# Performance work log

Measured on AMD Instinct MI355X. Metric: run time of the kernel, lower is better.

The kernel has to match this reference:

```python
import jax, jax.numpy as jnp
import numpy as np

N = 50000        # nodes
E = 1600000      # edges (avg degree 32)
CZ = 64          # c_z pair channel dim
STEPS = 3        # num_equilibration_steps
DITHER = 1e-4    # dither_eps in average_rotations


def quat_mul(a, b):
    # Hamilton product, quats as [w, x, y, z]
    aw, ax, ay, az = a[..., 0], a[..., 1], a[..., 2], a[..., 3]
    bw, bx, by, bz = b[..., 0], b[..., 1], b[..., 2], b[..., 3]
    return jnp.stack([
        aw * bw - ax * bx - ay * by - az * bz,
        aw * bx + ax * bw + ay * bz - az * by,
        aw * by - ax * bz + ay * bw + az * bx,
        aw * bz + ax * by - ay * bx + az * bw,
    ], axis=-1)


def quat_conj(q):
    return q * jnp.array([1.0, -1.0, -1.0, -1.0], q.dtype)


def quat_to_rot(q):
    w, x, y, z = q[..., 0], q[..., 1], q[..., 2], q[..., 3]
    r00 = 1 - 2 * (y * y + z * z); r01 = 2 * (x * y - w * z); r02 = 2 * (x * z + w * y)
    r10 = 2 * (x * y + w * z); r11 = 1 - 2 * (x * x + z * z); r12 = 2 * (y * z - w * x)
    r20 = 2 * (x * z - w * y); r21 = 2 * (y * z + w * x); r22 = 1 - 2 * (x * x + y * y)
    return jnp.stack([
        jnp.stack([r00, r01, r02], -1),
        jnp.stack([r10, r11, r12], -1),
        jnp.stack([r20, r21, r22], -1),
    ], axis=-2)


def rotmat_to_quat(R):
    # Branchless Shepperd method: 4 candidates, pick numerically best.
    m00, m01, m02 = R[..., 0, 0], R[..., 0, 1], R[..., 0, 2]
    m10, m11, m12 = R[..., 1, 0], R[..., 1, 1], R[..., 1, 2]
    m20, m21, m22 = R[..., 2, 0], R[..., 2, 1], R[..., 2, 2]
    q0 = jnp.stack([1 + m00 + m11 + m22, m21 - m12, m02 - m20, m10 - m01], -1)
    q1 = jnp.stack([m21 - m12, 1 + m00 - m11 - m22, m01 + m10, m02 + m20], -1)
    q2 = jnp.stack([m02 - m20, m01 + m10, 1 - m00 + m11 - m22, m12 + m21], -1)
    q3 = jnp.stack([m10 - m01, m02 + m20, m12 + m21, 1 - m00 - m11 + m22], -1)
    cand = jnp.stack([q0, q1, q2, q3], axis=-2)           # [N,4,4]
    scores = jnp.stack([m00 + m11 + m22, m00, m11, m22], -1)
    idx = jnp.argmax(scores, axis=-1)
    q = cand[jnp.arange(cand.shape[0]), idx]              # [N,4]
    q = q / jnp.linalg.norm(q, axis=-1, keepdims=True)
    return q * jnp.where(q[..., :1] < 0, -1.0, 1.0)      # canonical w >= 0


def rotmat_to_rotvec(R):
    q = rotmat_to_quat(R)
    w, v = q[..., 0], q[..., 1:]
    vn = jnp.linalg.norm(v, axis=-1)
    theta = 2.0 * jnp.arctan2(vn, w)
    small = vn < 1e-6
    safe = jnp.where(small, 1.0, vn)
    return jnp.where(small[..., None], 2.0 * v, (theta / safe)[..., None] * v)


def rotvec_to_quat(rotvec, eps=1e-8):
    theta = jnp.linalg.norm(rotvec + eps, axis=-1)
    omega = rotvec / theta[..., None]
    return jnp.concatenate([jnp.cos(theta / 2)[..., None],
                            jnp.sin(theta / 2)[..., None] * omega], axis=-1)


def setup_inputs() -> dict:
    key = jax.random.key(0)
    ks = jax.random.split(key, 8)
    return {
        "edge_features": jax.random.normal(ks[0], (E, CZ), jnp.float32),
        "quats": jax.random.normal(ks[1], (N, 4), jnp.float32),
        "trans": jax.random.normal(ks[2], (N, 3), jnp.float32) * 10.0,
        "W_update": jax.random.normal(ks[3], (CZ, 6), jnp.float32) * 0.02,
        "b_update": jax.random.normal(ks[4], (6,), jnp.float32) * 0.02,
        "W_logits": jax.random.normal(ks[5], (CZ, 1), jnp.float32) * 0.1,
        "b_logits": jax.random.normal(ks[6], (1,), jnp.float32) * 0.1,
        "edge_index": jax.random.randint(ks[7], (2, E), 0, N, jnp.int32),
    }


def reference(edge_features, quats, trans, W_update, b_update, W_logits, b_logits, edge_index):
    n = quats.shape[0]
    dst, src = edge_index[0], edge_index[1]

    # pairwise update vec + segment softmax weights over destination node (edge_index[1])
    q_upd = edge_features @ W_update + b_update              # [E,6]
    logits = edge_features @ W_logits + b_logits             # [E,1]
    seg_max = jax.ops.segment_max(logits, src, num_segments=n)
    seg_max = jnp.where(jnp.isfinite(seg_max), seg_max, 0.0)
    ex = jnp.exp(logits - seg_max[src])
    denom = jax.ops.segment_sum(ex, src, num_segments=n)
    weights = ex / (denom[src] + 1e-16)                      # [E,1]

    # relative rigid: inv(dst) o src
    qn = quats / jnp.linalg.norm(quats, axis=-1, keepdims=True)
    Rn = quat_to_rot(qn)                                     # [N,3,3]
    q_rel = quat_mul(quat_conj(qn[dst]), qn[src])            # [E,4]
    t_rel = jnp.einsum('eji,ej->ei', Rn[dst], trans[src] - trans[dst])  # R^T (t_s - t_d)

    # compose_q_update_vec (openfold): q' = q + q*(0,b,c,d), normalized; t' = t + R(q) t_vec
    bcd, tvec = q_upd[:, :3], q_upd[:, 3:]
    pair_q = q_rel + quat_mul(q_rel, jnp.concatenate([jnp.zeros_like(bcd[:, :1]), bcd], -1))
    pair_q = pair_q / jnp.linalg.norm(pair_q, axis=-1, keepdims=True)
    pair_t = t_rel + jnp.einsum('eij,ej->ei', quat_to_rot(q_rel), tvec)
    pair_R = quat_to_rot(pair_q)                             # [E,3,3]

    # equilibrate loop: scatter rotation averaging with SVD projection
    R, t = Rn, trans
    key = jax.random.key(42)
    for step in range(STEPS):
        dst_R, dst_t = R[dst], t[dst]
        R_pred = jnp.einsum('eij,ejk->eik', dst_R, pair_R)   # [E,3,3]
        R_sum = jax.ops.segment_sum((R_pred * weights[:, :, None]).reshape(-1, 9),
                                    src, num_segments=n).reshape(n, 3, 3)
        R_sum = R_sum + DITHER * jax.random.normal(jax.random.fold_in(key, step),
                                                   R_sum.shape, R_sum.dtype)
        U, S, Vh = jnp.linalg.svd(R_sum, full_matrices=False)
        d = jnp.linalg.det(U @ Vh)
        col = jnp.stack([jnp.ones_like(d), jnp.ones_like(d), d], -1)[:, None, :]
        R = U @ (Vh * col)                                   # proper rotation
        t_pred = dst_t + jnp.einsum('eij,ej->ei', dst_R, pair_t)
        t = jax.ops.segment_sum(t_pred * weights, src, num_segments=n)

    q_out = rotvec_to_quat(rotmat_to_rotvec(R))
    return jnp.concatenate([q_out, t], axis=-1)              # [N,7]
```

## Files before the change

kernel.cpp:

```cpp
#include <hip/hip_runtime.h>
#include <math.h>

#define TPB 256
#define SCAN_B 1024

__device__ __forceinline__ void quat_to_R(float w, float x, float y, float z, float* R) {
    R[0] = 1.f - 2.f*(y*y + z*z);
    R[1] = 2.f*(x*y - w*z);
    R[2] = 2.f*(x*z + w*y);
    R[3] = 2.f*(x*y + w*z);
    R[4] = 1.f - 2.f*(x*x + z*z);
    R[5] = 2.f*(y*z - w*x);
    R[6] = 2.f*(x*z - w*y);
    R[7] = 2.f*(y*z + w*x);
    R[8] = 1.f - 2.f*(x*x + y*y);
}

__device__ __forceinline__ float hsum32(float v) {
    #pragma unroll
    for (int o = 16; o > 0; o >>= 1) v += __shfl_xor(v, o);
    return v;
}
__device__ __forceinline__ float hmax32(float v) {
    #pragma unroll
    for (int o = 16; o > 0; o >>= 1) v = fmaxf(v, __shfl_xor(v, o));
    return v;
}

__global__ __launch_bounds__(TPB) void k_init(
    const float* __restrict__ quats, const float* __restrict__ trans,
    float* __restrict__ qn, float* __restrict__ RT, int* __restrict__ deg, int N)
{
    int n = blockIdx.x * TPB + threadIdx.x;
    if (n >= N) return;
    float4 q = ((const float4*)quats)[n];
    float inv = rsqrtf(q.x*q.x + q.y*q.y + q.z*q.z + q.w*q.w);
    float w = q.x*inv, x = q.y*inv, y = q.z*inv, z = q.w*inv;
    ((float4*)qn)[n] = make_float4(w, x, y, z);
    float R[9];
    quat_to_R(w, x, y, z, R);
    float t0 = trans[(size_t)n*3+0], t1 = trans[(size_t)n*3+1], t2 = trans[(size_t)n*3+2];
    float4* rt = (float4*)(RT + (size_t)n*12);
    rt[0] = make_float4(R[0], R[1], R[2], t0);
    rt[1] = make_float4(R[3], R[4], R[5], t1);
    rt[2] = make_float4(R[6], R[7], R[8], t2);
    deg[n] = 0;
}

__global__ __launch_bounds__(TPB) void k_hist(
    const int* __restrict__ ei, int* __restrict__ deg, int E)
{
    int e = blockIdx.x * TPB + threadIdx.x;
    if (e >= E) return;
    atomicAdd(deg + ei[(size_t)E + e], 1);
}

__global__ __launch_bounds__(SCAN_B) void k_scan1(
    const int* __restrict__ deg, int* __restrict__ row, int* __restrict__ bsum, int N)
{
    __shared__ int sh[SCAN_B];
    int i = blockIdx.x * SCAN_B + threadIdx.x;
    int v = (i < N) ? deg[i] : 0;
    sh[threadIdx.x] = v;
    __syncthreads();
    #pragma unroll
    for (int o = 1; o < SCAN_B; o <<= 1) {
        int t = (threadIdx.x >= o) ? sh[threadIdx.x - o] : 0;
        __syncthreads();
        sh[threadIdx.x] += t;
        __syncthreads();
    }
    if (i < N) row[i] = sh[threadIdx.x] - v;
    if (threadIdx.x == SCAN_B - 1) bsum[blockIdx.x] = sh[SCAN_B - 1];
}

__global__ __launch_bounds__(SCAN_B) void k_scan2(int* __restrict__ bsum, int nb)
{
    __shared__ int sh[SCAN_B];
    int v = (threadIdx.x < nb) ? bsum[threadIdx.x] : 0;
    sh[threadIdx.x] = v;
    __syncthreads();
    #pragma unroll
    for (int o = 1; o < SCAN_B; o <<= 1) {
        int t = (threadIdx.x >= o) ? sh[threadIdx.x - o] : 0;
        __syncthreads();
        sh[threadIdx.x] += t;
        __syncthreads();
    }
    if (threadIdx.x < nb) bsum[threadIdx.x] = sh[threadIdx.x] - v;
}

__global__ __launch_bounds__(TPB) void k_scan3(
    int* __restrict__ row, const int* __restrict__ bsum,
    int* __restrict__ cursor, int N, int E)
{
    int i = blockIdx.x * TPB + threadIdx.x;
    if (i >= N) return;
    int v = row[i] + bsum[i >> 10];
    row[i] = v;
    cursor[i] = v;
    if (i == 0) row[N] = E;
}

__global__ __launch_bounds__(TPB) void k_edge_pre(
    const float* __restrict__ ef, const int* __restrict__ ei,
    const float* __restrict__ qn, const float* __restrict__ trans,
    const float* __restrict__ Wu, const float* __restrict__ bu,
    const float* __restrict__ Wl, const float* __restrict__ bl,
    int* __restrict__ cursor, float4* __restrict__ pay, int E)
{
    __shared__ __align__(16) float Ws[7][64];
    __shared__ float accS[256][7];
    for (int i = threadIdx.x; i < 7*64; i += TPB) {
        int j = i >> 6, k = i & 63;
        Ws[j][k] = (j < 6) ? Wu[k*6 + j] : Wl[k];
    }
    __syncthreads();

    int tid = threadIdx.x;
    int sub = tid & 3, eL = tid >> 2;
    int blockStart = blockIdx.x * TPB;

    #pragma unroll
    for (int r = 0; r < 4; ++r) {
        int el = r * 64 + eL;
        int e = blockStart + el;
        float acc[7] = {0.f,0.f,0.f,0.f,0.f,0.f,0.f};
        if (e < E) {
            const float4* ef4 = (const float4*)(ef + (size_t)e * 64) + sub * 4;
            #pragma unroll
            for (int k = 0; k < 4; ++k) {
                float4 v = ef4[k];
                #pragma unroll
                for (int j = 0; j < 7; ++j) {
                    float4 w = ((const float4*)Ws[j])[sub*4 + k];
                    acc[j] = fmaf(v.x, w.x, fmaf(v.y, w.y, fmaf(v.z, w.z, fmaf(v.w, w.w, acc[j]))));
                }
            }
        }
        #pragma unroll
        for (int j = 0; j < 7; ++j) {
            acc[j] += __shfl_xor(acc[j], 1);
            acc[j] += __shfl_xor(acc[j], 2);
        }
        if (sub == 0) {
            #pragma unroll
            for (int j = 0; j < 7; ++j) accS[el][j] = acc[j];
        }
    }
    __syncthreads();

    int e = blockStart + tid;
    if (e >= E) return;
    float acc[7];
    #pragma unroll
    for (int j = 0; j < 7; ++j) acc[j] = accS[tid][j];
    #pragma unroll
    for (int j = 0; j < 6; ++j) acc[j] += bu[j];
    acc[6] += bl[0];

    int dst = ei[e];
    int src = ei[(size_t)E + e];
    float4 qd = ((const float4*)qn)[dst];
    float4 qs = ((const float4*)qn)[src];
    float aw = qd.x, ax = -qd.y, ay = -qd.z, az = -qd.w;
    float bw = qs.x, bx = qs.y, by = qs.z, bz = qs.w;
    float rw = aw*bw - ax*bx - ay*by - az*bz;
    float rx = aw*bx + ax*bw + ay*bz - az*by;
    float ry = aw*by - ax*bz + ay*bw + az*bx;
    float rz = aw*bz + ax*by - ay*bx + az*bw;
    float b0 = acc[0], b1 = acc[1], b2 = acc[2];
    float pw = rw - rx*b0 - ry*b1 - rz*b2;
    float px = rx + rw*b0 + ry*b2 - rz*b1;
    float py = ry + rw*b1 - rx*b2 + rz*b0;
    float pz = rz + rw*b2 + rx*b1 - ry*b0;
    float pinv = rsqrtf(pw*pw + px*px + py*py + pz*pz);
    pw *= pinv; px *= pinv; py *= pinv; pz *= pinv;
    float dx = trans[(size_t)src*3+0] - trans[(size_t)dst*3+0];
    float dy = trans[(size_t)src*3+1] - trans[(size_t)dst*3+1];
    float dz = trans[(size_t)src*3+2] - trans[(size_t)dst*3+2];
    float Rd[9];
    quat_to_R(qd.x, qd.y, qd.z, qd.w, Rd);
    float tr0 = Rd[0]*dx + Rd[3]*dy + Rd[6]*dz;
    float tr1 = Rd[1]*dx + Rd[4]*dy + Rd[7]*dz;
    float tr2 = Rd[2]*dx + Rd[5]*dy + Rd[8]*dz;
    float Rr[9];
    quat_to_R(rw, rx, ry, rz, Rr);
    float t3 = acc[3], t4 = acc[4], t5 = acc[5];
    float pt0 = tr0 + Rr[0]*t3 + Rr[1]*t4 + Rr[2]*t5;
    float pt1 = tr1 + Rr[3]*t3 + Rr[4]*t4 + Rr[5]*t5;
    float pt2 = tr2 + Rr[6]*t3 + Rr[7]*t4 + Rr[8]*t5;

    int pos = atomicAdd(cursor + src, 1);
    unsigned ub = (unsigned)dst | (pw < 0.f ? 0x80000000u : 0u);
    pay[2*(size_t)pos+0] = make_float4(px, py, pz, __uint_as_float(ub));
    pay[2*(size_t)pos+1] = make_float4(pt0, pt1, pt2, acc[6]);
}

__global__ __launch_bounds__(TPB) void k_node_softmax(
    const int* __restrict__ row, float4* __restrict__ pay, int N)
{
    int g = blockIdx.x * TPB + threadIdx.x;
    int node = g >> 5;
    int ln = threadIdx.x & 31;
    if (node >= N) return;
    int start = row[node], end = row[node + 1];
    float m = -INFINITY, s = 0.f;
    for (int i = start + ln; i < end; i += 32) {
        float l = pay[2*(size_t)i+1].w;
        float mn = fmaxf(m, l);
        s = s * expf(m - mn) + expf(l - mn);
        m = mn;
    }
    float M = hmax32(m);
    float sadj = (m == -INFINITY) ? 0.f : s * expf(m - M);
    float S = hsum32(sadj);
    float inv = 1.f / (S + 1e-16f);
    for (int i = start + ln; i < end; i += 32) {
        float4 v = pay[2*(size_t)i+1];
        v.w = expf(v.w - M) * inv;
        pay[2*(size_t)i+1] = v;
    }
}

__global__ __launch_bounds__(TPB) void k_node_iter(
    const int* __restrict__ row, const float4* __restrict__ pay,
    const float* __restrict__ RT, float* __restrict__ RS, int N)
{
    int g = blockIdx.x * TPB + threadIdx.x;
    int node = g >> 5;
    int ln = threadIdx.x & 31;
    if (node >= N) return;
    int start = row[node], end = row[node + 1];

    float a00=0,a01=0,a02=0,a10=0,a11=0,a12=0,a20=0,a21=0,a22=0,s0=0,s1=0,s2=0;
    for (int i = start + ln; i < end; i += 32) {
        float4 q  = pay[2*(size_t)i+0];
        float4 tl = pay[2*(size_t)i+1];
        unsigned ub = __float_as_uint(q.w);
        int dst = (int)(ub & 0x7fffffffu);
        float s2q = q.x*q.x + q.y*q.y + q.z*q.z;
        float pw = sqrtf(fmaxf(0.f, 1.f - s2q));
        if (ub & 0x80000000u) pw = -pw;
        float w = tl.w;
        float P[9];
        quat_to_R(pw, q.x, q.y, q.z, P);
        const float4* rt = (const float4*)(RT + (size_t)dst * 12);
        float4 r0 = rt[0], r1 = rt[1], r2 = rt[2];
        a00 += w * (r0.x*P[0] + r0.y*P[3] + r0.z*P[6]);
        a01 += w * (r0.x*P[1] + r0.y*P[4] + r0.z*P[7]);
        a02 += w * (r0.x*P[2] + r0.y*P[5] + r0.z*P[8]);
        a10 += w * (r1.x*P[0] + r1.y*P[3] + r1.z*P[6]);
        a11 += w * (r1.x*P[1] + r1.y*P[4] + r1.z*P[7]);
        a12 += w * (r1.x*P[2] + r1.y*P[5] + r1.z*P[8]);
        a20 += w * (r2.x*P[0] + r2.y*P[3] + r2.z*P[6]);
        a21 += w * (r2.x*P[1] + r2.y*P[4] + r2.z*P[7]);
        a22 += w * (r2.x*P[2] + r2.y*P[5] + r2.z*P[8]);
        s0 += w * (r0.w + r0.x*tl.x + r0.y*tl.y + r0.z*tl.z);
        s1 += w * (r1.w + r1.x*tl.x + r1.y*tl.y + r1.z*tl.z);
        s2 += w * (r2.w + r2.x*tl.x + r2.y*tl.y + r2.z*tl.z);
    }
    a00 = hsum32(a00); a01 = hsum32(a01); a02 = hsum32(a02);
    a10 = hsum32(a10); a11 = hsum32(a11); a12 = hsum32(a12);
    a20 = hsum32(a20); a21 = hsum32(a21); a22 = hsum32(a22);
    s0 = hsum32(s0); s1 = hsum32(s1); s2 = hsum32(s2);
    if (ln == 0) {
        float4* rs = (float4*)(RS + (size_t)node * 12);
        rs[0] = make_float4(a00, a01, a02, s0);
        rs[1] = make_float4(a10, a11, a12, s1);
        rs[2] = make_float4(a20, a21, a22, s2);
    }
}

#define JROT(SPP,SQQ,SPQ,SPR,SQR, VP0,VP1,VP2, VQ0,VQ1,VQ2) do { \
    float apq_ = SPQ; \
    if (fabsf(apq_) > 1e-30f) { \
        float tau_ = (SQQ - SPP) / (2.0f * apq_); \
        float tt_ = copysignf(1.0f, tau_) / (fabsf(tau_) + sqrtf(1.0f + tau_*tau_)); \
        float c_ = 1.0f / sqrtf(1.0f + tt_*tt_); \
        float s_ = tt_ * c_; \
        SPP -= tt_ * apq_; SQQ += tt_ * apq_; SPQ = 0.0f; \
        float pr_ = SPR, qr_ = SQR; \
        SPR = c_*pr_ - s_*qr_; SQR = s_*pr_ + c_*qr_; \
        float a_, b_; \
        a_ = VP0; b_ = VQ0; VP0 = c_*a_ - s_*b_; VQ0 = s_*a_ + c_*b_; \
        a_ = VP1; b_ = VQ1; VP1 = c_*a_ - s_*b_; VQ1 = s_*a_ + c_*b_; \
        a_ = VP2; b_ = VQ2; VP2 = c_*a_ - s_*b_; VQ2 = s_*a_ + c_*b_; \
    } \
} while (0)

#define CSW(LA,LB, A0,A1,A2, B0,B1,B2) do { \
    if (LB > LA) { float t_; \
        t_=LA; LA=LB; LB=t_; \
        t_=A0; A0=B0; B0=t_; \
        t_=A1; A1=B1; B1=t_; \
        t_=A2; A2=B2; B2=t_; } \
} while (0)

__global__ __launch_bounds__(TPB) void k_node_project(
    float* __restrict__ RT, const float* __restrict__ RS, int N)
{
    int n = blockIdx.x * TPB + threadIdx.x;
    if (n >= N) return;
    const float4* rs = (const float4*)(RS + (size_t)n * 12);
    float4 q0 = rs[0], q1 = rs[1], q2 = rs[2];
    float A[9] = {q0.x, q0.y, q0.z, q1.x, q1.y, q1.z, q2.x, q2.y, q2.z};
    float t0 = q0.w, t1 = q1.w, t2 = q2.w;

    float s00 = A[0]*A[0] + A[3]*A[3] + A[6]*A[6];
    float s11 = A[1]*A[1] + A[4]*A[4] + A[7]*A[7];
    float s22 = A[2]*A[2] + A[5]*A[5] + A[8]*A[8];
    float s01 = A[0]*A[1] + A[3]*A[4] + A[6]*A[7];
    float s02 = A[0]*A[2] + A[3]*A[5] + A[6]*A[8];
    float s12 = A[1]*A[2] + A[4]*A[5] + A[7]*A[8];
    float v00=1.f,v01=0.f,v02=0.f, v10=0.f,v11=1.f,v12=0.f, v20=0.f,v21=0.f,v22=1.f;
    #pragma unroll
    for (int sweep = 0; sweep < 8; ++sweep) {
        JROT(s00,s11,s01, s02,s12, v00,v10,v20, v01,v11,v21);
        JROT(s00,s22,s02, s01,s12, v00,v10,v20, v02,v12,v22);
        JROT(s11,s22,s12, s01,s02, v01,v11,v21, v02,v12,v22);
    }
    CSW(s00,s11, v00,v10,v20, v01,v11,v21);
    CSW(s00,s22, v00,v10,v20, v02,v12,v22);
    CSW(s11,s22, v01,v11,v21, v02,v12,v22);

    float u0x = A[0]*v00 + A[1]*v10 + A[2]*v20;
    float u0y = A[3]*v00 + A[4]*v10 + A[5]*v20;
    float u0z = A[6]*v00 + A[7]*v10 + A[8]*v20;
    float n0 = sqrtf(u0x*u0x + u0y*u0y + u0z*u0z);
    if (n0 > 1e-20f) { float r = 1.0f/n0; u0x*=r; u0y*=r; u0z*=r; }
    else { u0x = 1.f; u0y = 0.f; u0z = 0.f; }
    float u1x = A[0]*v01 + A[1]*v11 + A[2]*v21;
    float u1y = A[3]*v01 + A[4]*v11 + A[5]*v21;
    float u1z = A[6]*v01 + A[7]*v11 + A[8]*v21;
    float d01 = u1x*u0x + u1y*u0y + u1z*u0z;
    u1x -= d01*u0x; u1y -= d01*u0y; u1z -= d01*u0z;
    float n1 = sqrtf(u1x*u1x + u1y*u1y + u1z*u1z);
    if (n1 > 1e-12f) { float r = 1.0f/n1; u1x*=r; u1y*=r; u1z*=r; }
    else {
        float hx = (fabsf(u0x) < 0.9f) ? 1.f : 0.f;
        float hy = 1.f - hx;
        float cx = -u0z*hy, cy = u0z*hx, cz = u0x*hy - u0y*hx;
        float cn = rsqrtf(cx*cx + cy*cy + cz*cz);
        u1x = cx*cn; u1y = cy*cn; u1z = cz*cn;
    }
    float u2x = u0y*u1z - u0z*u1y;
    float u2y = u0z*u1x - u0x*u1z;
    float u2z = u0x*u1y - u0y*u1x;
    float detV = v00*(v11*v22 - v12*v21) - v01*(v10*v22 - v12*v20) + v02*(v10*v21 - v11*v20);
    if (detV < 0.f) { v02 = -v02; v12 = -v12; v22 = -v22; }
    float4* rt = (float4*)(RT + (size_t)n * 12);
    rt[0] = make_float4(u0x*v00 + u1x*v01 + u2x*v02,
                        u0x*v10 + u1x*v11 + u2x*v12,
                        u0x*v20 + u1x*v21 + u2x*v22, t0);
    rt[1] = make_float4(u0y*v00 + u1y*v01 + u2y*v02,
                        u0y*v10 + u1y*v11 + u2y*v12,
                        u0y*v20 + u1y*v21 + u2y*v22, t1);
    rt[2] = make_float4(u0z*v00 + u1z*v01 + u2z*v02,
                        u0z*v10 + u1z*v11 + u2z*v12,
                        u0z*v20 + u1z*v21 + u2z*v22, t2);
}

__global__ __launch_bounds__(TPB) void k_finalize(
    const float* __restrict__ RT, float* __restrict__ out, int N)
{
    int n = blockIdx.x * TPB + threadIdx.x;
    if (n >= N) return;
    const float4* rt = (const float4*)(RT + (size_t)n * 12);
    float4 r0 = rt[0], r1 = rt[1], r2 = rt[2];
    float m00 = r0.x, m01 = r0.y, m02 = r0.z;
    float m10 = r1.x, m11 = r1.y, m12 = r1.z;
    float m20 = r2.x, m21 = r2.y, m22 = r2.z;
    float tr = m00 + m11 + m22;
    int idx = 0; float best = tr;
    if (m00 > best) { best = m00; idx = 1; }
    if (m11 > best) { best = m11; idx = 2; }
    if (m22 > best) { best = m22; idx = 3; }
    float qw, qx, qy, qz;
    if (idx == 0)      { qw = 1.f+m00+m11+m22; qx = m21-m12;        qy = m02-m20;        qz = m10-m01; }
    else if (idx == 1) { qw = m21-m12;         qx = 1.f+m00-m11-m22; qy = m01+m10;       qz = m02+m20; }
    else if (idx == 2) { qw = m02-m20;         qx = m01+m10;        qy = 1.f-m00+m11-m22; qz = m12+m21; }
    else               { qw = m10-m01;         qx = m02+m20;        qy = m12+m21;        qz = 1.f-m00-m11+m22; }
    float inv = rsqrtf(qw*qw + qx*qx + qy*qy + qz*qz);
    qw *= inv; qx *= inv; qy *= inv; qz *= inv;
    if (qw < 0.f) { qw = -qw; qx = -qx; qy = -qy; qz = -qz; }
    float vn = sqrtf(qx*qx + qy*qy + qz*qz);
    float theta = 2.f * atan2f(vn, qw);
    float r0v, r1v, r2v;
    if (vn < 1e-6f) { r0v = 2.f*qx; r1v = 2.f*qy; r2v = 2.f*qz; }
    else { float s = theta / vn; r0v = s*qx; r1v = s*qy; r2v = s*qz; }
    float e0 = r0v + 1e-8f, e1 = r1v + 1e-8f, e2 = r2v + 1e-8f;
    float th2 = sqrtf(e0*e0 + e1*e1 + e2*e2);
    float half = 0.5f * th2;
    float cw = cosf(half), sw = sinf(half);
    float it = 1.0f / th2;
    out[(size_t)n*7+0] = cw;
    out[(size_t)n*7+1] = sw * r0v * it;
    out[(size_t)n*7+2] = sw * r1v * it;
    out[(size_t)n*7+3] = sw * r2v * it;
    out[(size_t)n*7+4] = r0.w;
    out[(size_t)n*7+5] = r1.w;
    out[(size_t)n*7+6] = r2.w;
}

extern "C" void kernel_launch(void* const* d_in, const int* in_sizes, int n_in,
                              void* d_out, int out_size, void* d_ws, size_t ws_size,
                              hipStream_t stream)
{
    (void)n_in; (void)out_size; (void)ws_size;
    const float* ef    = (const float*)d_in[0];
    const float* quats = (const float*)d_in[1];
    const float* trans = (const float*)d_in[2];
    const float* Wu    = (const float*)d_in[3];
    const float* bu    = (const float*)d_in[4];
    const float* Wl    = (const float*)d_in[5];
    const float* bl    = (const float*)d_in[6];
    const int*   ei    = (const int*)d_in[7];
    float* out = (float*)d_out;

    const int N = in_sizes[1] / 4;
    const int E = in_sizes[7] / 2;

    float* ws = (float*)d_ws;
    size_t off = 0;
    float*  qn   = ws + off; off += (size_t)4*N;
    float4* pay  = (float4*)(ws + off); off += (size_t)8*E;
    float*  RT   = ws + off; off += (size_t)12*N;
    float*  RS   = ws + off; off += (size_t)12*N;
    int* deg    = (int*)(ws + off); off += (size_t)N;
    int* row    = (int*)(ws + off); off += (size_t)(N + 1);
    int* bsum   = (int*)(ws + off); off += (size_t)SCAN_B;

    int nodeBlocks = (N + TPB - 1) / TPB;
    int edgeBlocks = (E + TPB - 1) / TPB;
    int halfBlocks = (int)(((size_t)N * 32 + TPB - 1) / TPB);
    int scanBlocks = (N + SCAN_B - 1) / SCAN_B;

    k_init<<<nodeBlocks, TPB, 0, stream>>>(quats, trans, qn, RT, deg, N);
    k_hist<<<edgeBlocks, TPB, 0, stream>>>(ei, deg, E);
    k_scan1<<<scanBlocks, SCAN_B, 0, stream>>>(deg, row, bsum, N);
    k_scan2<<<1, SCAN_B, 0, stream>>>(bsum, scanBlocks);
    k_scan3<<<nodeBlocks, TPB, 0, stream>>>(row, bsum, deg, N, E);
    k_edge_pre<<<edgeBlocks, TPB, 0, stream>>>(ef, ei, qn, trans, Wu, bu, Wl, bl,
                                               deg, pay, E);
    k_node_softmax<<<halfBlocks, TPB, 0, stream>>>(row, pay, N);
    for (int s = 0; s < 3; ++s) {
        k_node_iter<<<halfBlocks, TPB, 0, stream>>>(row, pay, RT, RS, N);
        k_node_project<<<nodeBlocks, TPB, 0, stream>>>(RT, RS, N);
    }
    k_finalize<<<nodeBlocks, TPB, 0, stream>>>(RT, out, N);
}
```

Before: 358.4 us.

## Split logits/weights into separate arrays and use 8 lanes per node in iter

After: 378.6 us. 1.06x slower.

```diff
diff --git a/kernel.cpp b/kernel.cpp
--- a/kernel.cpp
+++ b/kernel.cpp
@@ -24,6 +24,12 @@
 __device__ __forceinline__ float hmax32(float v) {
     #pragma unroll
     for (int o = 16; o > 0; o >>= 1) v = fmaxf(v, __shfl_xor(v, o));
+    return v;
+}
+__device__ __forceinline__ float hsum8(float v) {
+    v += __shfl_xor(v, 4);
+    v += __shfl_xor(v, 2);
+    v += __shfl_xor(v, 1);
     return v;
 }
 
@@ -107,7 +113,8 @@
     const float* __restrict__ qn, const float* __restrict__ trans,
     const float* __restrict__ Wu, const float* __restrict__ bu,
     const float* __restrict__ Wl, const float* __restrict__ bl,
-    int* __restrict__ cursor, float4* __restrict__ pay, int E)
+    int* __restrict__ cursor, float4* __restrict__ pay,
+    float* __restrict__ lg, int E)
 {
     __shared__ __align__(16) float Ws[7][64];
     __shared__ float accS[256][7];
@@ -194,11 +201,13 @@
     int pos = atomicAdd(cursor + src, 1);
     unsigned ub = (unsigned)dst | (pw < 0.f ? 0x80000000u : 0u);
     pay[2*(size_t)pos+0] = make_float4(px, py, pz, __uint_as_float(ub));
-    pay[2*(size_t)pos+1] = make_float4(pt0, pt1, pt2, acc[6]);
+    pay[2*(size_t)pos+1] = make_float4(pt0, pt1, pt2, 0.f);
+    lg[pos] = acc[6];
 }
 
 __global__ __launch_bounds__(TPB) void k_node_softmax(
-    const int* __restrict__ row, float4* __restrict__ pay, int N)
+    const int* __restrict__ row, const float* __restrict__ lg,
+    float* __restrict__ wgt, int N)
 {
     int g = blockIdx.x * TPB + threadIdx.x;
     int node = g >> 5;
@@ -207,7 +216,7 @@
     int start = row[node], end = row[node + 1];
     float m = -INFINITY, s = 0.f;
     for (int i = start + ln; i < end; i += 32) {
-        float l = pay[2*(size_t)i+1].w;
+        float l = lg[i];
         float mn = fmaxf(m, l);
         s = s * expf(m - mn) + expf(l - mn);
         m = mn;
@@ -217,32 +226,31 @@
     float S = hsum32(sadj);
     float inv = 1.f / (S + 1e-16f);
     for (int i = start + ln; i < end; i += 32) {
-        float4 v = pay[2*(size_t)i+1];
-        v.w = expf(v.w - M) * inv;
-        pay[2*(size_t)i+1] = v;
+        wgt[i] = expf(lg[i] - M) * inv;
     }
 }
 
 __global__ __launch_bounds__(TPB) void k_node_iter(
     const int* __restrict__ row, const float4* __restrict__ pay,
+    const float* __restrict__ wgt,
     const float* __restrict__ RT, float* __restrict__ RS, int N)
 {
     int g = blockIdx.x * TPB + threadIdx.x;
-    int node = g >> 5;
-    int ln = threadIdx.x & 31;
+    int node = g >> 3;
+    int ln = threadIdx.x & 7;
     if (node >= N) return;
     int start = row[node], end = row[node + 1];
 
     float a00=0,a01=0,a02=0,a10=0,a11=0,a12=0,a20=0,a21=0,a22=0,s0=0,s1=0,s2=0;
-    for (int i = start + ln; i < end; i += 32) {
+    for (int i = start + ln; i < end; i += 8) {
         float4 q  = pay[2*(size_t)i+0];
         float4 tl = pay[2*(size_t)i+1];
+        float w = wgt[i];
         unsigned ub = __float_as_uint(q.w);
         int dst = (int)(ub & 0x7fffffffu);
         float s2q = q.x*q.x + q.y*q.y + q.z*q.z;
         float pw = sqrtf(fmaxf(0.f, 1.f - s2q));
         if (ub & 0x80000000u) pw = -pw;
-        float w = tl.w;
         float P[9];
         quat_to_R(pw, q.x, q.y, q.z, P);
         const float4* rt = (const float4*)(RT + (size_t)dst * 12);
@@ -260,10 +268,10 @@
         s1 += w * (r1.w + r1.x*tl.x + r1.y*tl.y + r1.z*tl.z);
         s2 += w * (r2.w + r2.x*tl.x + r2.y*tl.y + r2.z*tl.z);
     }
-    a00 = hsum32(a00); a01 = hsum32(a01); a02 = hsum32(a02);
-    a10 = hsum32(a10); a11 = hsum32(a11); a12 = hsum32(a12);
-    a20 = hsum32(a20); a21 = hsum32(a21); a22 = hsum32(a22);
-    s0 = hsum32(s0); s1 = hsum32(s1); s2 = hsum32(s2);
+    a00 = hsum8(a00); a01 = hsum8(a01); a02 = hsum8(a02);
+    a10 = hsum8(a10); a11 = hsum8(a11); a12 = hsum8(a12);
+    a20 = hsum8(a20); a21 = hsum8(a21); a22 = hsum8(a22);
+    s0 = hsum8(s0); s1 = hsum8(s1); s2 = hsum8(s2);
     if (ln == 0) {
         float4* rs = (float4*)(RS + (size_t)node * 12);
         rs[0] = make_float4(a00, a01, a02, s0);
@@ -425,6 +433,8 @@
     size_t off = 0;
     float*  qn   = ws + off; off += (size_t)4*N;
     float4* pay  = (float4*)(ws + off); off += (size_t)8*E;
+    float*  lg   = ws + off; off += (size_t)E;
+    float*  wgt  = ws + off; off += (size_t)E;
     float*  RT   = ws + off; off += (size_t)12*N;
     float*  RS   = ws + off; off += (size_t)12*N;
     int* deg    = (int*)(ws + off); off += (size_t)N;
@@ -433,7 +443,8 @@
 
     int nodeBlocks = (N + TPB - 1) / TPB;
     int edgeBlocks = (E + TPB - 1) / TPB;
-    int halfBlocks = (int)(((size_t)N * 32 + TPB - 1) / TPB);
+    int halfBlocks  = (int)(((size_t)N * 32 + TPB - 1) / TPB);
+    int octBlocks   = (int)(((size_t)N * 8 + TPB - 1) / TPB);
     int scanBlocks = (N + SCAN_B - 1) / SCAN_B;
 
     k_init<<<nodeBlocks, TPB, 0, stream>>>(quats, trans, qn, RT, deg, N);
@@ -442,10 +453,10 @@
     k_scan2<<<1, SCAN_B, 0, stream>>>(bsum, scanBlocks);
     k_scan3<<<nodeBlocks, TPB, 0, stream>>>(row, bsum, deg, N, E);
     k_edge_pre<<<edgeBlocks, TPB, 0, stream>>>(ef, ei, qn, trans, Wu, bu, Wl, bl,
-                                               deg, pay, E);
-    k_node_softmax<<<halfBlocks, TPB, 0, stream>>>(row, pay, N);
+                                               deg, pay, lg, E);
+    k_node_softmax<<<halfBlocks, TPB, 0, stream>>>(row, lg, wgt, N);
     for (int s = 0; s < 3; ++s) {
-        k_node_iter<<<halfBlocks, TPB, 0, stream>>>(row, pay, RT, RS, N);
+        k_node_iter<<<octBlocks, TPB, 0, stream>>>(row, pay, wgt, RT, RS, N);
         k_node_project<<<nodeBlocks, TPB, 0, stream>>>(RT, RS, N);
     }
     k_finalize<<<nodeBlocks, TPB, 0, stream>>>(RT, out, N);
```
